# Kernel tuning notes

Measured on AMD Instinct MI355X. Metric: run time of the kernel, lower is better.

## Reference

```python
import jax, jax.numpy as jnp
import numpy as np

THRESH = 0.3
VRESET = 0.0
TAU_M = 3.0
MAX_D = 5
LENS = 0.5  # surrogate-gradient window half-width

B, WIN, N_IN = 512, 100, 700
H1, H2, H3 = 512, 256, 128

@jax.custom_vjp
def spike_fn(mem):
    # Heaviside spike with rectangular surrogate gradient (standard ActFun in SNN repos)
    return (mem > THRESH).astype(mem.dtype)

def _spike_fwd(mem):
    return spike_fn(mem), mem

def _spike_bwd(mem, g):
    return (g * (jnp.abs(mem - THRESH) < LENS).astype(g.dtype),)

spike_fn.defvjp(_spike_fwd, _spike_bwd)


def mem_update(i_spike, o_spike, mem, W, alpha):
    # mem = mem*alpha*(1-o_spike) + W @ i_spike - o_spike*vreset
    mem = mem * alpha * (1.0 - o_spike) + i_spike @ W.T - o_spike * VRESET
    s = spike_fn(mem)
    mem = mem * (mem < THRESH).astype(mem.dtype)  # hard reset above threshold
    return mem, s


def setup_inputs() -> dict:
    key = jax.random.key(0)
    ks = jax.random.split(key, 7)
    x = (jax.random.uniform(ks[0], (B, WIN, N_IN), jnp.float32) > 0.9).astype(jnp.float32)

    def lin(k, fan_out, fan_in):
        bound = 1.0 / np.sqrt(fan_in)
        return jax.random.uniform(k, (fan_out, fan_in), jnp.float32, -bound, bound)

    return {
        "x": x,
        "W_ih1": lin(ks[1], H1, N_IN),
        "W_h1h2": lin(ks[2], H2, H1),
        "W_h2h3": lin(ks[3], H3, H2),
        "W_h3h2": lin(ks[4], H2, H3),
        "W_h2h1": lin(ks[5], H1, H2),
        "W_h1o": lin(ks[6], N_IN, H1),
    }


def reference(x, W_ih1, W_h1h2, W_h2h3, W_h3h2, W_h2h1, W_h1o):
    b, t, n = x.shape
    alpha = jnp.exp(jnp.asarray(-1.0 / TAU_M, x.dtype))
    ext = jnp.concatenate([jnp.zeros((b, MAX_D, n), x.dtype), x], axis=1)  # [B, T+max_d, N]
    xs = jnp.swapaxes(ext, 0, 1)  # [T+max_d, B, N]

    z = lambda d: jnp.zeros((b, d), x.dtype)
    carry0 = (z(H1), z(H1), z(H2), z(H2), z(H3), z(H3),
              z(H2), z(H2), z(H1), z(H1), z(n), z(n))

    def step(carry, xt):
        m1, s1, m2, s2, m3, s3, m2d, s2d, m1d, s1d, mo, so = carry
        m1, s1 = mem_update(xt, s1, m1, W_ih1, alpha)
        m2, s2 = mem_update(s1, s2, m2, W_h1h2, alpha)
        m3, s3 = mem_update(s2, s3, m3, W_h2h3, alpha)
        m2d, s2d = mem_update(s3, s2d, m2d, W_h3h2, alpha)
        m1d, s1d = mem_update(s2d, s1d, m1d, W_h2h1, alpha)
        mo, so = mem_update(s1d, so, mo, W_h1o, alpha)
        return (m1, s1, m2, s2, m3, s3, m2d, s2d, m1d, s1d, mo, so), so

    _, all_o = jax.lax.scan(step, carry0, xs)  # [T+max_d, B, N]
    return jnp.swapaxes(all_o[MAX_D:], 0, 1)   # [B, T, N]
```

## Files before the change

### kernel.cpp

```cpp
#include <hip/hip_runtime.h>
#include <cmath>

namespace {

constexpr int kWin = 100;
constexpr int kNin = 700;

constexpr size_t OFF1 = 0;
constexpr size_t OFF2 = 358400;
constexpr size_t OFF3 = 489472;
constexpr size_t OFF4 = 522240;
constexpr size_t OFF5 = 555008;
constexpr size_t OFF6 = 686080;
constexpr size_t OFF_END = 1044480;
constexpr size_t XM_OFF_U64 = OFF_END / 2;

__global__ void transpose_k(const float* __restrict__ src, float* __restrict__ dst,
                            int H, int K) {
  int idx = blockIdx.x * blockDim.x + threadIdx.x;
  if (idx < H * K) {
    int h = idx / K;
    int k = idx - h * K;
    dst[k * H + h] = src[idx];
  }
}

__global__ __launch_bounds__(256) void xmask_k(const float* __restrict__ x,
                                               unsigned long long* __restrict__ xm) {
  const int bid = blockIdx.x;
  const int tid = threadIdx.x;
  const int lane = tid & 63;
  const int wv = tid >> 6;
  const float* xr = x + (size_t)bid * kNin;
  unsigned long long* dst = xm + (size_t)bid * 12;
#pragma unroll
  for (int s = 0; s < 3; ++s) {
    const int h = s * 256 + tid;
    const bool p = (h < kNin) ? (xr[h] != 0.0f) : false;
    const unsigned long long b = __ballot(p);
    if (lane == 0) dst[s * 4 + wv] = b;
  }
}

template <int K, int H, bool BUILD, typename FCh>
__device__ __forceinline__ void lif(const float* __restrict__ WT, FCh&& chunk,
                                    double* mem, unsigned long long* mOut,
                                    double (*part)[3][256],
                                    float* outRow,
                                    int kp, int ht, int lane, int wv4,
                                    double alpha) {
  constexpr int NS = (H + 255) / 256;
  constexpr int NC = (K + 31) / 32;
  double acc[NS];
#pragma unroll
  for (int s = 0; s < NS; ++s) acc[s] = 0.0;

  for (int c = kp; c < NC; c += 4) {
    unsigned m = __builtin_amdgcn_readfirstlane(chunk(c));
    const float* __restrict__ cbase = WT + (size_t)c * 32 * H;
    const int cnt = __builtin_popcount(m);
    int i = 0;
    for (; i + 4 <= cnt; i += 4) {
      const int b0 = __builtin_ctz(m); m &= m - 1;
      const int b1 = __builtin_ctz(m); m &= m - 1;
      const int b2 = __builtin_ctz(m); m &= m - 1;
      const int b3 = __builtin_ctz(m); m &= m - 1;
      const float* p0 = cbase + b0 * H;
      const float* p1 = cbase + b1 * H;
      const float* p2 = cbase + b2 * H;
      const float* p3 = cbase + b3 * H;
#pragma unroll
      for (int s = 0; s < NS; ++s) {
        constexpr bool kFull = true;
        (void)kFull;
        const int h = s * 256 + ht;
        if ((s + 1) * 256 <= H || h < H) {
          const float f0 = p0[h];
          const float f1 = p1[h];
          const float f2 = p2[h];
          const float f3 = p3[h];
          acc[s] += (double)f0;
          acc[s] += (double)f1;
          acc[s] += (double)f2;
          acc[s] += (double)f3;
        }
      }
    }
    for (; i < cnt; ++i) {
      const int b0 = __builtin_ctz(m); m &= m - 1;
      const float* p0 = cbase + b0 * H;
#pragma unroll
      for (int s = 0; s < NS; ++s) {
        const int h = s * 256 + ht;
        if ((s + 1) * 256 <= H || h < H) acc[s] += (double)p0[h];
      }
    }
  }

#pragma unroll
  for (int s = 0; s < NS; ++s) part[kp][s][ht] = acc[s];
  __syncthreads();

  bool pred[NS];
#pragma unroll
  for (int s = 0; s < NS; ++s) {
    const int h = s * 256 + ht;
    if ((s + 1) * 256 <= H || h < H) {
      const double p01 = part[0][s][ht] + part[1][s][ht];
      const double tot = (p01 + part[2][s][ht]) + part[3][s][ht];
      const double mm = mem[s] * alpha + tot;
      pred[s] = (mm > 0.3);
      mem[s] = (mm < 0.3) ? mm : 0.0;
      if (!BUILD) {
        if (kp == s) outRow[h] = pred[s] ? 1.0f : 0.0f;
      }
    } else {
      pred[s] = false;
    }
  }
  if (BUILD) {
#pragma unroll
    for (int s = 0; s < NS; ++s) {
      const unsigned long long b = __ballot(pred[s]);
      if (kp == 0 && lane == 0) mOut[s * 4 + wv4] = b;
    }
    __syncthreads();
  }
}

__global__ __launch_bounds__(1024, 8) void snn_main(
    const float* __restrict__ wsf, const unsigned long long* __restrict__ xmask,
    float* __restrict__ out) {
  const int tid = threadIdx.x;
  const int kp = tid >> 8;
  const int ht = tid & 255;
  const int lane = tid & 63;
  const int wv4 = (tid >> 6) & 3;
  const int row = blockIdx.x;

  const float* WT1 = wsf + OFF1;
  const float* WT2 = wsf + OFF2;
  const float* WT3 = wsf + OFF3;
  const float* WT4 = wsf + OFF4;
  const float* WT5 = wsf + OFF5;
  const float* WT6 = wsf + OFF6;

  __shared__ unsigned long long mk[2][12];
  __shared__ double parts[2][4][3][256];

  double m1[2] = {0.0, 0.0};
  double m2[1] = {0.0};
  double m3[1] = {0.0};
  double m4[1] = {0.0};
  double m5[2] = {0.0, 0.0};
  double m6[3] = {0.0, 0.0, 0.0};

  const double alpha = exp(-1.0 / 3.0);

  const unsigned long long* xmRow = xmask + (size_t)row * kWin * 12;
  float* outRowBase = out + (size_t)row * kWin * kNin;

  for (int t = 0; t < kWin; ++t) {
    const unsigned* xm32 = (const unsigned*)(xmRow + (size_t)t * 12);
    const unsigned* mk0 = (const unsigned*)&mk[0][0];
    const unsigned* mk1 = (const unsigned*)&mk[1][0];

    lif<700, 512, true>(WT1, [&](int c) { return xm32[c]; }, m1, mk[0],
                        parts[0], nullptr, kp, ht, lane, wv4, alpha);
    lif<512, 256, true>(WT2, [&](int c) { return mk0[c]; }, m2, mk[1],
                        parts[1], nullptr, kp, ht, lane, wv4, alpha);
    lif<256, 128, true>(WT3, [&](int c) { return mk1[c]; }, m3, mk[0],
                        parts[0], nullptr, kp, ht, lane, wv4, alpha);
    lif<128, 256, true>(WT4, [&](int c) { return mk0[c]; }, m4, mk[1],
                        parts[1], nullptr, kp, ht, lane, wv4, alpha);
    lif<256, 512, true>(WT5, [&](int c) { return mk1[c]; }, m5, mk[0],
                        parts[0], nullptr, kp, ht, lane, wv4, alpha);
    float* outRow = outRowBase + (size_t)t * kNin;
    lif<512, 700, false>(WT6, [&](int c) { return mk0[c]; }, m6, nullptr,
                         parts[1], outRow, kp, ht, lane, wv4, alpha);
  }
}

}

extern "C" void kernel_launch(void* const* d_in, const int* in_sizes, int n_in,
                              void* d_out, int out_size, void* d_ws, size_t ws_size,
                              hipStream_t stream) {
  const float* x = (const float*)d_in[0];
  float* ws = (float*)d_ws;
  unsigned long long* xm = (unsigned long long*)d_ws + XM_OFF_U64;
  float* out = (float*)d_out;

  struct TK { int H, K; size_t off; int idx; };
  const TK tk[6] = {
      {512, 700, OFF1, 1},
      {256, 512, OFF2, 2},
      {128, 256, OFF3, 3},
      {256, 128, OFF4, 4},
      {512, 256, OFF5, 5},
      {700, 512, OFF6, 6},
  };
  for (int i = 0; i < 6; ++i) {
    const int n = tk[i].H * tk[i].K;
    transpose_k<<<(n + 255) / 256, 256, 0, stream>>>(
        (const float*)d_in[tk[i].idx], ws + tk[i].off, tk[i].H, tk[i].K);
  }

  xmask_k<<<512 * kWin, 256, 0, stream>>>(x, xm);

  snn_main<<<512, 1024, 0, stream>>>(ws, xm, out);
}
```

Baseline: 1.125 ms.

## Assign one neuron per thread and drop split-K shared-memory reduction

Restructures the per-layer LIF update so each thread owns one output neuron and walks every input chunk itself, using 64-bit spike masks. This removes the 4-way K split, the double-precision partial-sum buffer in shared memory, and one of the two barriers per layer. The block shrinks from 1024 to 704 threads. In exchange each thread does a longer serial gather with less parallelism per neuron, and some waves sit idle on narrow layers.

```diff
diff --git a/kernel.cpp b/kernel.cpp
--- a/kernel.cpp
+++ b/kernel.cpp
@@ -42,100 +42,73 @@
   }
 }
 
-template <int K, int H, bool BUILD, typename FCh>
-__device__ __forceinline__ void lif(const float* __restrict__ WT, FCh&& chunk,
-                                    double* mem, unsigned long long* mOut,
-                                    double (*part)[3][256],
-                                    float* outRow,
-                                    int kp, int ht, int lane, int wv4,
-                                    double alpha) {
-  constexpr int NS = (H + 255) / 256;
-  constexpr int NC = (K + 31) / 32;
-  double acc[NS];
+template <int K, int H, bool OUT>
+__device__ __forceinline__ void lif(const float* __restrict__ WT,
+                                    const unsigned* __restrict__ mwIn,
+                                    unsigned long long* mkNext,
+                                    double& mem, double alpha,
+                                    float* __restrict__ outRow,
+                                    int tid, int lane, int wv) {
+  constexpr int NC = (K + 63) / 64;
+  const bool waveOn = (wv * 64 < H);
+  if (waveOn) {
+    unsigned long long mloc[NC];
 #pragma unroll
-  for (int s = 0; s < NS; ++s) acc[s] = 0.0;
-
-  for (int c = kp; c < NC; c += 4) {
-    unsigned m = __builtin_amdgcn_readfirstlane(chunk(c));
-    const float* __restrict__ cbase = WT + (size_t)c * 32 * H;
-    const int cnt = __builtin_popcount(m);
-    int i = 0;
-    for (; i + 4 <= cnt; i += 4) {
-      const int b0 = __builtin_ctz(m); m &= m - 1;
-      const int b1 = __builtin_ctz(m); m &= m - 1;
-      const int b2 = __builtin_ctz(m); m &= m - 1;
-      const int b3 = __builtin_ctz(m); m &= m - 1;
-      const float* p0 = cbase + b0 * H;
-      const float* p1 = cbase + b1 * H;
-      const float* p2 = cbase + b2 * H;
-      const float* p3 = cbase + b3 * H;
-#pragma unroll
-      for (int s = 0; s < NS; ++s) {
-        constexpr bool kFull = true;
-        (void)kFull;
-        const int h = s * 256 + ht;
-        if ((s + 1) * 256 <= H || h < H) {
-          const float f0 = p0[h];
-          const float f1 = p1[h];
-          const float f2 = p2[h];
-          const float f3 = p3[h];
-          acc[s] += (double)f0;
-          acc[s] += (double)f1;
-          acc[s] += (double)f2;
-          acc[s] += (double)f3;
+    for (int c = 0; c < NC; ++c) {
+      const unsigned lo = __builtin_amdgcn_readfirstlane(mwIn[2 * c]);
+      const unsigned hi = __builtin_amdgcn_readfirstlane(mwIn[2 * c + 1]);
+      mloc[c] = ((unsigned long long)hi << 32) | lo;
+    }
+    bool sp = false;
+    const bool active = (tid < H);
+    if (active) {
+      double a0 = 0.0, a1 = 0.0, a2 = 0.0, a3 = 0.0;
+      const float* __restrict__ cb = WT + tid;
+#pragma unroll 1
+      for (int c = 0; c < NC; ++c) {
+        unsigned long long m = mloc[c];
+        const float* __restrict__ cb2 = cb + (size_t)c * 64 * H;
+        const int cnt = __popcll(m);
+        int i = 0;
+        for (; i + 4 <= cnt; i += 4) {
+          const int b0 = (int)__builtin_ctzll(m); m &= m - 1;
+          const int b1 = (int)__builtin_ctzll(m); m &= m - 1;
+          const int b2 = (int)__builtin_ctzll(m); m &= m - 1;
+          const int b3 = (int)__builtin_ctzll(m); m &= m - 1;
+          const float f0 = cb2[b0 * H];
+          const float f1 = cb2[b1 * H];
+          const float f2 = cb2[b2 * H];
+          const float f3 = cb2[b3 * H];
+          a0 += (double)f0;
+          a1 += (double)f1;
+          a2 += (double)f2;
+          a3 += (double)f3;
+        }
+        for (; i < cnt; ++i) {
+          const int b = (int)__builtin_ctzll(m); m &= m - 1;
+          a0 += (double)cb2[b * H];
         }
       }
+      const double sum = (a0 + a1) + (a2 + a3);
+      const double mm = mem * alpha + sum;
+      sp = (mm > 0.3);
+      mem = (mm < 0.3) ? mm : 0.0;
+      if (OUT) outRow[tid] = sp ? 1.0f : 0.0f;
     }
-    for (; i < cnt; ++i) {
-      const int b0 = __builtin_ctz(m); m &= m - 1;
-      const float* p0 = cbase + b0 * H;
-#pragma unroll
-      for (int s = 0; s < NS; ++s) {
-        const int h = s * 256 + ht;
-        if ((s + 1) * 256 <= H || h < H) acc[s] += (double)p0[h];
-      }
+    if (!OUT) {
+      const unsigned long long b = __ballot(sp);
+      if (lane == 0) mkNext[wv] = b;
     }
   }
-
-#pragma unroll
-  for (int s = 0; s < NS; ++s) part[kp][s][ht] = acc[s];
   __syncthreads();
-
-  bool pred[NS];
-#pragma unroll
-  for (int s = 0; s < NS; ++s) {
-    const int h = s * 256 + ht;
-    if ((s + 1) * 256 <= H || h < H) {
-      const double p01 = part[0][s][ht] + part[1][s][ht];
-      const double tot = (p01 + part[2][s][ht]) + part[3][s][ht];
-      const double mm = mem[s] * alpha + tot;
-      pred[s] = (mm > 0.3);
-      mem[s] = (mm < 0.3) ? mm : 0.0;
-      if (!BUILD) {
-        if (kp == s) outRow[h] = pred[s] ? 1.0f : 0.0f;
-      }
-    } else {
-      pred[s] = false;
-    }
-  }
-  if (BUILD) {
-#pragma unroll
-    for (int s = 0; s < NS; ++s) {
-      const unsigned long long b = __ballot(pred[s]);
-      if (kp == 0 && lane == 0) mOut[s * 4 + wv4] = b;
-    }
-    __syncthreads();
-  }
 }
 
-__global__ __launch_bounds__(1024, 8) void snn_main(
+__global__ __launch_bounds__(704) void snn_main(
     const float* __restrict__ wsf, const unsigned long long* __restrict__ xmask,
     float* __restrict__ out) {
   const int tid = threadIdx.x;
-  const int kp = tid >> 8;
-  const int ht = tid & 255;
   const int lane = tid & 63;
-  const int wv4 = (tid >> 6) & 3;
+  const int wv = tid >> 6;
   const int row = blockIdx.x;
 
   const float* WT1 = wsf + OFF1;
@@ -146,14 +119,8 @@
   const float* WT6 = wsf + OFF6;
 
   __shared__ unsigned long long mk[2][12];
-  __shared__ double parts[2][4][3][256];
 
-  double m1[2] = {0.0, 0.0};
-  double m2[1] = {0.0};
-  double m3[1] = {0.0};
-  double m4[1] = {0.0};
-  double m5[2] = {0.0, 0.0};
-  double m6[3] = {0.0, 0.0, 0.0};
+  double m1 = 0.0, m2 = 0.0, m3 = 0.0, m4 = 0.0, m5 = 0.0, m6 = 0.0;
 
   const double alpha = exp(-1.0 / 3.0);
 
@@ -162,22 +129,18 @@
 
   for (int t = 0; t < kWin; ++t) {
     const unsigned* xm32 = (const unsigned*)(xmRow + (size_t)t * 12);
-    const unsigned* mk0 = (const unsigned*)&mk[0][0];
-    const unsigned* mk1 = (const unsigned*)&mk[1][0];
 
-    lif<700, 512, true>(WT1, [&](int c) { return xm32[c]; }, m1, mk[0],
-                        parts[0], nullptr, kp, ht, lane, wv4, alpha);
-    lif<512, 256, true>(WT2, [&](int c) { return mk0[c]; }, m2, mk[1],
-                        parts[1], nullptr, kp, ht, lane, wv4, alpha);
-    lif<256, 128, true>(WT3, [&](int c) { return mk1[c]; }, m3, mk[0],
-                        parts[0], nullptr, kp, ht, lane, wv4, alpha);
-    lif<128, 256, true>(WT4, [&](int c) { return mk0[c]; }, m4, mk[1],
-                        parts[1], nullptr, kp, ht, lane, wv4, alpha);
-    lif<256, 512, true>(WT5, [&](int c) { return mk1[c]; }, m5, mk[0],
-                        parts[0], nullptr, kp, ht, lane, wv4, alpha);
-    float* outRow = outRowBase + (size_t)t * kNin;
-    lif<512, 700, false>(WT6, [&](int c) { return mk0[c]; }, m6, nullptr,
-                         parts[1], outRow, kp, ht, lane, wv4, alpha);
+    lif<700, 512, false>(WT1, xm32, mk[0], m1, alpha, nullptr, tid, lane, wv);
+    lif<512, 256, false>(WT2, (const unsigned*)mk[0], mk[1], m2, alpha, nullptr,
+                         tid, lane, wv);
+    lif<256, 128, false>(WT3, (const unsigned*)mk[1], mk[0], m3, alpha, nullptr,
+                         tid, lane, wv);
+    lif<128, 256, false>(WT4, (const unsigned*)mk[0], mk[1], m4, alpha, nullptr,
+                         tid, lane, wv);
+    lif<256, 512, false>(WT5, (const unsigned*)mk[1], mk[0], m5, alpha, nullptr,
+                         tid, lane, wv);
+    lif<512, 700, true>(WT6, (const unsigned*)mk[0], nullptr, m6, alpha,
+                        outRowBase + (size_t)t * kNin, tid, lane, wv);
   }
 }
 
@@ -208,5 +171,5 @@
 
   xmask_k<<<512 * kWin, 256, 0, stream>>>(x, xm);
 
-  snn_main<<<512, 1024, 0, stream>>>(ws, xm, out);
+  snn_main<<<512, 704, 0, stream>>>(ws, xm, out);
 }
```

Result: slower. 2.830 ms (+151.6%).
